# Kernel optimization log

Hardware: AMD Instinct MI355X
Metric: run time of the kernel (lower is better)

## Reference

```python
import jax, jax.numpy as jnp
import numpy as np

D_MODEL, EMB_DIM, MLP_ORDER, SEQ_LEN, BATCH = 768, 3, 16, 8192, 8


def setup_inputs() -> dict:
    key = jax.random.key(0)
    ks = jax.random.split(key, 12)
    L = SEQ_LEN
    # PositionalEmbedding buffers (deterministic, as in __init__)
    t = jnp.linspace(0.0, 1.0, L)[None, :, None]                      # [1, L, 1]
    bands = (EMB_DIM - 1) // 2                                        # = 1
    t_long = jnp.linspace(0.0, L - 1.0, L)[None, :, None]
    w = 2.0 * jnp.pi * t_long / L
    f = jnp.linspace(1e-4, bands - 1.0, bands)[None, None]
    zc = jnp.exp(-1j * f * w)
    z = jnp.concatenate([t, zc.real, zc.imag], axis=-1).astype(jnp.float32)  # [1, L, 3]
    # ExponentialModulation deltas (deterministic)
    max_decay = jnp.log(0.01) / 0.3
    min_decay = jnp.log(0.01) / 1.5
    deltas = jnp.linspace(min_decay, max_decay, D_MODEL)[None, None].astype(jnp.float32)  # [1,1,D]
    s = 0.1
    return {
        "x": jax.random.normal(ks[0], (BATCH, D_MODEL, L), jnp.float32),
        "L": L,
        "z": z,
        "t": t.astype(jnp.float32),
        "deltas": deltas,
        "freq": jnp.ones((1, MLP_ORDER), jnp.float32),
        "W0": jax.random.normal(ks[1], (EMB_DIM, MLP_ORDER), jnp.float32) * s,
        "b0": jax.random.normal(ks[2], (MLP_ORDER,), jnp.float32) * s,
        "W1": jax.random.normal(ks[3], (MLP_ORDER, MLP_ORDER), jnp.float32) * s,
        "b1": jax.random.normal(ks[4], (MLP_ORDER,), jnp.float32) * s,
        "W2": jax.random.normal(ks[5], (MLP_ORDER, MLP_ORDER), jnp.float32) * s,
        "b2": jax.random.normal(ks[6], (MLP_ORDER,), jnp.float32) * s,
        "W3": jax.random.normal(ks[7], (MLP_ORDER, D_MODEL), jnp.float32) * s,
        "b3": jax.random.normal(ks[8], (D_MODEL,), jnp.float32) * s,
        "bias": jax.random.normal(ks[9], (D_MODEL,), jnp.float32),
    }


def reference(x, L, z, t, deltas, freq, W0, b0, W1, b1, W2, b2, W3, b3, bias):
    # filter generation: MLP with shared Sin activation, then exponential modulation
    zl = z[:, :L]
    h = jnp.sin(freq * (zl @ W0 + b0))
    h = jnp.sin(freq * (h @ W1 + b1))
    h = jnp.sin(freq * (h @ W2 + b2))
    h = h @ W3 + b3                               # [1, L, D]
    h = h * jnp.exp(-t[:, :L] * jnp.abs(deltas))  # exponential modulation
    k = h[0].T                                    # [D, L]
    # fftconv: causal long convolution via zero-padded FFT + skip x*bias
    fft_size = 2 * L
    y = jnp.fft.irfft(jnp.fft.rfft(x, n=fft_size) * jnp.fft.rfft(k, n=fft_size), n=fft_size)[..., :L]
    return y + x * bias[:, None]
```

## Files before the change

### kernel.cpp

```cpp
#include <hip/hip_runtime.h>
#include <math.h>


#define LSEQ 8192
#define NCH 768
#define NBATCH 8
#define NT 512

#define OFF_TWB  0
#define OFF_TW16 1024
#define OFF_TL   5124
#define OFF_TWC  6660
#define OFF_H    10240
#define OFF_KF   141312

__device__ __forceinline__ float2 cadd(float2 a, float2 b){ return make_float2(a.x+b.x, a.y+b.y); }
__device__ __forceinline__ float2 csub(float2 a, float2 b){ return make_float2(a.x-b.x, a.y-b.y); }
__device__ __forceinline__ float2 cmul(float2 a, float2 b){ return make_float2(a.x*b.x - a.y*b.y, a.x*b.y + a.y*b.x); }
__device__ __forceinline__ float2 mni(float2 a){ return make_float2(a.y, -a.x); }

__device__ __forceinline__ void wave_sync(){
    asm volatile("s_waitcnt lgkmcnt(0)" ::: "memory");
}
__device__ __forceinline__ void fence(){
    asm volatile("" ::: "memory");
}

__device__ __forceinline__ int IDX(int i){ return i ^ (((i>>4) ^ (i>>8)) & 15); }
__device__ __forceinline__ int drev(int k){
    return ((k & 15) << 9) | (((k >> 4) & 15) << 5) | (((k >> 8) & 15) << 1) | (k >> 12);
}

#define C1 0.923879532511286756f
#define S1 0.382683432365089772f
#define R2 0.707106781186547524f

template<bool FULL>
__device__ __forceinline__ void dft16(float2 q[16]) {
    if constexpr (FULL) {
#pragma unroll
        for (int j = 0; j < 8; ++j) { float2 u=q[j], v=q[j+8]; q[j]=cadd(u,v); q[j+8]=csub(u,v); }
    }
    q[9]  = cmul(q[9],  make_float2( C1,-S1));
    q[10] = cmul(q[10], make_float2( R2,-R2));
    q[11] = cmul(q[11], make_float2( S1,-C1));
    q[12] = mni(q[12]);
    q[13] = cmul(q[13], make_float2(-S1,-C1));
    q[14] = cmul(q[14], make_float2(-R2,-R2));
    q[15] = cmul(q[15], make_float2(-C1,-S1));
#pragma unroll
    for (int b = 0; b < 16; b += 8) {
#pragma unroll
        for (int j = 0; j < 4; ++j) { float2 u=q[b+j], v=q[b+j+4]; q[b+j]=cadd(u,v); q[b+j+4]=csub(u,v); }
        q[b+5] = cmul(q[b+5], make_float2( R2,-R2));
        q[b+6] = mni(q[b+6]);
        q[b+7] = cmul(q[b+7], make_float2(-R2,-R2));
    }
#pragma unroll
    for (int b = 0; b < 16; b += 4) {
        float2 u0=q[b], v0=q[b+2], u1=q[b+1], v1=q[b+3];
        q[b]=cadd(u0,v0); q[b+2]=csub(u0,v0);
        q[b+1]=cadd(u1,v1); q[b+3]=mni(csub(u1,v1));
    }
#pragma unroll
    for (int b = 0; b < 16; b += 2) { float2 u=q[b], v=q[b+1]; q[b]=cadd(u,v); q[b+1]=csub(u,v); }
}

template<int PASS>
__device__ __forceinline__ int psb(int t) {
    if constexpr (PASS == 0) {
        return t ^ (((t>>4) ^ (t>>8)) & 15);
    } else if constexpr (PASS == 1) {
        int p = t & 31, hb = t >> 5;
        return ((hb<<9) | p) ^ (((p>>4) ^ (hb<<1)) & 15);
    } else {
        int h = t >> 1;
        return ((h<<5) | (t&1)) ^ (((h<<1) ^ (h>>3)) & 15);
    }
}
template<int PASS>
__device__ __forceinline__ int paddr(int sb, int r) {
    if constexpr (PASS == 0)      return (sb ^ (2*(r&7))) + (r<<9);
    else if constexpr (PASS == 1) return (sb ^ ((2*(r&7)) ^ (r>>3))) + (r<<5);
    else                          return sb ^ ((r<<1) ^ (r>>3));
}

template<int PASS, bool DIT, bool PRUNED>
__device__ __forceinline__ void r16p(float2* lds, const float2 (*twT)[68], int t) {
    static constexpr int RV[16] = {0,8,4,12,2,10,6,14,1,9,5,13,3,11,7,15};
    const int sb = psb<PASS>(t);
    int rL, rH = 0;
    if constexpr (PASS == 0) { rL = 32 + (t & 31); rH = (t >> 5) << 1; }
    else if constexpr (PASS == 1) { rL = t & 31; }
    else { rL = 64 + (t & 1); }
    float2 q[16];
    if constexpr (PRUNED) {
#pragma unroll
        for (int r = 0; r < 8; ++r) { q[r] = lds[paddr<PASS>(sb, r)]; q[r+8] = q[r]; }
    } else {
#pragma unroll
        for (int r = 0; r < 16; ++r) q[r] = lds[paddr<PASS>(sb, r)];
    }
    if constexpr (DIT) {
#pragma unroll
        for (int m = 1; m < 16; ++m) {
            float2 w = twT[m][rL];
            if constexpr (PASS == 0) w = cmul(w, twT[m][rH]);
            q[m] = cmul(q[m], w);
        }
        dft16<true>(q);
    } else {
        dft16<!PRUNED>(q);
#pragma unroll
        for (int m = 1; m < 16; ++m) {
            float2 w = twT[m][rL];
            if constexpr (PASS == 0) w = cmul(w, twT[m][rH]);
            q[RV[m]] = cmul(q[RV[m]], w);
        }
    }
#pragma unroll
    for (int m = 0; m < 16; ++m) lds[paddr<PASS>(sb, m)] = q[RV[m]];
}

template<int PASS, bool DIT, bool PRUNED>
__device__ __forceinline__ void r16pp(float2* l0, float2* l1, const float2 (*twT)[68], int t) {
    r16p<PASS, DIT, PRUNED>(l0, twT, t);
    fence();
    r16p<PASS, DIT, PRUNED>(l1, twT, t);
}

__device__ __forceinline__ void load_twT(float2 (*twT)[68], const float* __restrict__ ws, int tid) {
    const float2* gTWB = (const float2*)(ws + OFF_TWB);
    const float2* gTL  = (const float2*)(ws + OFF_TL);
    const float2* gTWC = (const float2*)(ws + OFF_TWC);
    for (int idx = tid; idx < 16*66; idx += NT) {
        int r = idx >> 4, m = idx & 15;
        float2 v;
        if (r < 32)      v = gTWB[(r << 4) + m];
        else if (r < 64) v = gTL[((r - 32) << 4) + m];
        else             v = gTWC[((r - 64) << 4) + m];
        twT[m][r] = v;
    }
}

__device__ __forceinline__ void specpair(float2 V1, float2 V2, float4 kv, float2 W,
                                         float2& o1, float2& o2) {
    float2 Eh = make_float2(V1.x + V2.x, V1.y - V2.y);
    float2 Oh = make_float2(V1.y + V2.y, V2.x - V1.x);
    float2 S = make_float2(kv.x, kv.y);
    float a = W.x*kv.z, b = W.y*kv.w, cc = W.x*kv.w, dd = W.y*kv.z;
    float2 T  = make_float2(a - b, cc + dd);
    float2 T2 = make_float2(a + b, cc - dd);
    float2 Ep = cadd(cmul(Eh, S), cmul(Oh, T));
    float2 Op = cadd(cmul(Eh, T2), cmul(Oh, S));
    o1 = make_float2(Ep.y + Op.x, Ep.x - Op.y);
    o2 = make_float2(Op.x - Ep.y, Ep.x + Op.y);
}

__device__ __forceinline__ void spec_rows(float2* l, int pA, int pB,
                                          float4 kvk, float4 kvj, float2 W, float2 Wj) {
    float2 uA = l[pA], vA = l[pA^1];
    float2 uB = l[pB], vB = l[pB^1];
    float2 Vk = cadd(uA, vA), Vk4 = csub(uA, vA);
    float2 Vj = cadd(uB, vB), Vj4 = csub(uB, vB);
    float2 r1, r2, r1j, r2j;
    specpair(Vk, Vj4, kvk, W,  r1,  r2);
    specpair(Vj, Vk4, kvj, Wj, r1j, r2j);
    l[pA]   = cadd(r1, r2j);  l[pA^1] = csub(r1, r2j);
    l[pB]   = cadd(r1j, r2);  l[pB^1] = csub(r1j, r2);
}

__device__ __forceinline__ void spec_dc(float2* l, float4 kv) {
    float2 u = l[0], v = l[1];
    float2 V0 = cadd(u, v), VN = csub(u, v);
    float U0 = V0.x + V0.y, UL = V0.x - V0.y;
    float re = U0*kv.x + UL*kv.y;
    float im = U0*kv.x - UL*kv.y;
    float2 s0 = make_float2(im, re);
    float2 P = make_float2(VN.x*kv.z + VN.y*kv.w, VN.x*kv.w - VN.y*kv.z);
    float2 s1 = make_float2(-P.y, P.x);
    l[0] = cadd(s0, s1);
    l[1] = csub(s0, s1);
}

__device__ __forceinline__ void filt_store(float2* l, float4* kf, int k, int jj,
                                           int pA, int pB, float2 W, float2 Wj,
                                           float sc, float eb) {
    float2 uA = l[pA], vA = l[pA^1];
    float2 uB = l[pB], vB = l[pB^1];
    float2 Vk = cadd(uA, vA), Vk4 = csub(uA, vA);
    float2 Vj = cadd(uB, vB), Vj4 = csub(uB, vB);
    {
        float2 E = make_float2(Vk.x + Vj4.x + eb, Vk.y - Vj4.y);
        float2 O = make_float2(Vk.y + Vj4.y, Vj4.x - Vk.x);
        float2 D = cmul(W, O);
        kf[k] = make_float4(E.x*sc, E.y*sc, D.x*sc, D.y*sc);
    }
    {
        float2 E = make_float2(Vj.x + Vk4.x + eb, Vj.y - Vk4.y);
        float2 O = make_float2(Vj.y + Vk4.y, Vk4.x - Vj.x);
        float2 D = cmul(Wj, O);
        kf[jj] = make_float4(E.x*sc, E.y*sc, D.x*sc, D.y*sc);
    }
}
__device__ __forceinline__ void filt_dc(float2* l, float4* kf, float bc) {
    float2 u = l[0], v = l[1];
    float2 V0 = cadd(u, v), VN = csub(u, v);
    kf[0] = make_float4((V0.x + V0.y + bc)/16384.f, (V0.x - V0.y + bc)/16384.f,
                        (VN.x + bc)/8192.f, -VN.y/8192.f);
}

__global__ __launch_bounds__(512) void k_pre(const float* __restrict__ z, const float* __restrict__ freq,
        const float* __restrict__ W0, const float* __restrict__ b0,
        const float* __restrict__ W1, const float* __restrict__ b1,
        const float* __restrict__ W2, const float* __restrict__ b2,
        float* __restrict__ ws, float* __restrict__ H) {
    __shared__ double2 lA[128], lB[128];
    const int t = threadIdx.x;
    if (blockIdx.x == 0) {
        const double K = -2.0 * 3.14159265358979323846 / 16384.0;
        if (t < 128)      { double a = K * (double)(t << 7); lA[t] = make_double2(cos(a), sin(a)); }
        else if (t < 256) { int b = t - 128; double a = K * (double)b; lB[b] = make_double2(cos(a), sin(a)); }
        __syncthreads();
        auto wf = [&](int e) -> float2 {
            e &= 16383;
            double2 A = lA[e >> 7], B = lB[e & 127];
            return make_float2((float)(A.x*B.x - A.y*B.y), (float)(A.x*B.y + A.y*B.x));
        };
        float2* tw16 = (float2*)(ws + OFF_TW16);
        for (int k = t; k <= 2048; k += 512) tw16[k] = wf(k);
        if (t < 32) {
            float2* rowL = (float2*)(ws + OFF_TL)  + (t << 4);
            float2* rowB = (float2*)(ws + OFF_TWB) + (t << 4);
#pragma unroll
            for (int m = 0; m < 16; ++m) { rowL[m] = wf(2*t*m); rowB[m] = wf(32*t*m); }
        } else if (t < 34) {
            int c2 = t - 32;
            float2* rowC = (float2*)(ws + OFF_TWC) + (c2 << 4);
#pragma unroll
            for (int m = 0; m < 16; ++m) rowC[m] = wf(512*c2*m);
        }
    } else {
        const int j = ((blockIdx.x - 1) << 9) + t;
        const float z0 = z[j*3+0], z1 = z[j*3+1], z2 = z[j*3+2];
        float h[16], g[16];
#pragma unroll
        for (int m = 0; m < 16; ++m)
            h[m] = sinf(freq[m] * (z0*W0[m] + z1*W0[16+m] + z2*W0[32+m] + b0[m]));
#pragma unroll
        for (int m = 0; m < 16; ++m) {
            float a = b1[m];
#pragma unroll
            for (int p = 0; p < 16; ++p) a += h[p] * W1[p*16+m];
            g[m] = sinf(freq[m] * a);
        }
#pragma unroll
        for (int m = 0; m < 16; ++m) {
            float a = b2[m];
#pragma unroll
            for (int p = 0; p < 16; ++p) a += g[p] * W2[p*16+m];
            h[m] = sinf(freq[m] * a);
        }
        float4* hp = (float4*)(H + (j << 4));
        hp[0] = make_float4(h[0],  h[1],  h[2],  h[3]);
        hp[1] = make_float4(h[4],  h[5],  h[6],  h[7]);
        hp[2] = make_float4(h[8],  h[9],  h[10], h[11]);
        hp[3] = make_float4(h[12], h[13], h[14], h[15]);
    }
}

__global__ __launch_bounds__(NT) void k_filter(const float* __restrict__ H, const float* __restrict__ t,
        const float* __restrict__ deltas, const float* __restrict__ W3,
        const float* __restrict__ b3, const float* __restrict__ bias,
        const float* __restrict__ ws, float* __restrict__ KfF) {
    __shared__ float2 lds2[2][LSEQ];
    __shared__ float2 twT[16][68];
    const int c0 = blockIdx.x << 1, c1 = c0 + 1;
    const int tid = threadIdx.x;
    float2* l0 = lds2[0];
    float2* l1 = lds2[1];
    load_twT(twT, ws, tid);
    float w30[16], w31[16];
#pragma unroll
    for (int m = 0; m < 16; ++m) { w30[m] = W3[m*NCH + c0]; w31[m] = W3[m*NCH + c1]; }
    const float b30 = b3[c0], b31 = b3[c1];
    const float ad0 = fabsf(deltas[c0]), ad1 = fabsf(deltas[c1]);
    const float bc0 = bias[c0], bc1 = bias[c1];
    const int sbA = psb<0>(tid);
#pragma unroll 1
    for (int j = 0; j < 8; ++j) {
        int n = tid + (j << 9);
        const float4* hp = (const float4*)(H + (n << 5));
        float sA0 = b30, sB0 = b30, sA1 = b31, sB1 = b31;
#pragma unroll
        for (int q = 0; q < 4; ++q) {
            float4 a = hp[q];
            float4 b = hp[4+q];
            sA0 += a.x*w30[4*q] + a.y*w30[4*q+1] + a.z*w30[4*q+2] + a.w*w30[4*q+3];
            sB0 += b.x*w30[4*q] + b.y*w30[4*q+1] + b.z*w30[4*q+2] + b.w*w30[4*q+3];
            sA1 += a.x*w31[4*q] + a.y*w31[4*q+1] + a.z*w31[4*q+2] + a.w*w31[4*q+3];
            sB1 += b.x*w31[4*q] + b.y*w31[4*q+1] + b.z*w31[4*q+2] + b.w*w31[4*q+3];
        }
        float2 tv = ((const float2*)t)[n];
        int a0 = (sbA ^ (2*j)) + (j<<9);
        l0[a0] = make_float2(sA0 * expf(-tv.x*ad0), sB0 * expf(-tv.y*ad0));
        l1[a0] = make_float2(sA1 * expf(-tv.x*ad1), sB1 * expf(-tv.y*ad1));
    }
    __syncthreads();
    r16pp<0,false,true >(l0, l1, twT, tid); __syncthreads();
    r16pp<1,false,false>(l0, l1, twT, tid); wave_sync();
    r16pp<2,false,false>(l0, l1, twT, tid); __syncthreads();

    float4* kf0 = (float4*)KfF + (size_t)c0 * 4096;
    float4* kf1 = (float4*)KfF + (size_t)c1 * 4096;
    const float2* tw16 = (const float2*)(ws + OFF_TW16);
    const float sc = 1.0f / 32768.0f;
#pragma unroll 1
    for (int it = 0; it < 4; ++it) {
        int k  = tid + 1 + (it << 9);
        int jj = 4096 - k;
        int pA = IDX(drev(k)), pB = IDX(drev(jj));
        float2 W  = tw16[k];
        float2 Wj = make_float2(-W.y, -W.x);
        filt_store(l0, kf0, k, jj, pA, pB, W, Wj, sc, 2.0f*bc0);
        filt_store(l1, kf1, k, jj, pA, pB, W, Wj, sc, 2.0f*bc1);
    }
    if (tid == 0) { filt_dc(l0, kf0, bc0); filt_dc(l1, kf1, bc1); }
}

__global__ __launch_bounds__(NT) void k_main(const float* __restrict__ x, const float* __restrict__ ws,
        const float* __restrict__ KfF, float* __restrict__ out) {
    __shared__ float2 lds2[2][LSEQ];
    __shared__ float2 twT[16][68];
    const int bid = blockIdx.x;
    const int c = bid >> 1, half = bid & 1;
    const int tt = threadIdx.x;
    float2* l0 = lds2[0];
    float2* l1 = lds2[1];
    const float4* kf4 = (const float4*)KfF + (size_t)c * 4096;
    const float2* tw16 = (const float2*)(ws + OFF_TW16);
    const size_t rowstride = (size_t)NCH * LSEQ;
    const float* xbase = x + (size_t)(half*4) * rowstride + (size_t)c * LSEQ;
    float* obase = out + (size_t)(half*4) * rowstride + (size_t)c * LSEQ;

    const int EB = (tt << 1) ^ (((tt>>3) ^ (tt>>7)) & 15);

    load_twT(twT, ws, tt);

#pragma unroll 1
    for (int pp = 0; pp < 2; ++pp) {
        const float4* xr0 = (const float4*)(xbase + (size_t)(2*pp)     * rowstride);
        const float4* xr1 = (const float4*)(xbase + (size_t)(2*pp + 1) * rowstride);
#pragma unroll
        for (int j = 0; j < 4; ++j) {
            float4 v0 = xr0[tt + (j<<9)];
            float4 v1 = xr1[tt + (j<<9)];
            int a0 = (EB ^ (j<<2)) + (j<<10);
            l0[a0]   = make_float2(v0.x, v0.y);
            l0[a0^1] = make_float2(v0.z, v0.w);
            l1[a0]   = make_float2(v1.x, v1.y);
            l1[a0^1] = make_float2(v1.z, v1.w);
        }
        __syncthreads();
        r16pp<0,false,true >(l0, l1, twT, tt); __syncthreads();
        r16pp<1,false,false>(l0, l1, twT, tt); wave_sync();
        r16pp<2,false,false>(l0, l1, twT, tt); __syncthreads();

#pragma unroll 1
        for (int it = 0; it < 4; ++it) {
            int k  = tt + 1 + (it << 9);
            int jj = 4096 - k;
            int pA = IDX(drev(k)), pB = IDX(drev(jj));
            float4 kvk = kf4[k], kvj = kf4[jj];
            float2 W  = tw16[k];
            float2 Wj = make_float2(-W.y, -W.x);
            spec_rows(l0, pA, pB, kvk, kvj, W, Wj);
            spec_rows(l1, pA, pB, kvk, kvj, W, Wj);
        }
        if (tt == 0) {
            float4 kv = kf4[0];
            spec_dc(l0, kv);
            spec_dc(l1, kv);
        }
        __syncthreads();

        r16pp<2,true,false>(l0, l1, twT, tt); wave_sync();
        r16pp<1,true,false>(l0, l1, twT, tt); __syncthreads();
        r16pp<0,true,false>(l0, l1, twT, tt); __syncthreads();

        float4* o0 = (float4*)(obase + (size_t)(2*pp)     * rowstride);
        float4* o1 = (float4*)(obase + (size_t)(2*pp + 1) * rowstride);
#pragma unroll
        for (int j = 0; j < 4; ++j) {
            int a0 = (EB ^ (j<<2)) + (j<<10);
            float2 wA0 = l0[a0], wB0 = l0[a0^1];
            float2 wA1 = l1[a0], wB1 = l1[a0^1];
            o0[tt + (j<<9)] = make_float4(wA0.y, wA0.x, wB0.y, wB0.x);
            o1[tt + (j<<9)] = make_float4(wA1.y, wA1.x, wB1.y, wB1.x);
        }
        if (pp == 0) __syncthreads();
    }
}

extern "C" void kernel_launch(void* const* d_in, const int* in_sizes, int n_in,
                              void* d_out, int out_size, void* d_ws, size_t ws_size,
                              hipStream_t stream) {
    const float* x      = (const float*)d_in[0];
    const float* z      = (const float*)d_in[2];
    const float* t      = (const float*)d_in[3];
    const float* deltas = (const float*)d_in[4];
    const float* freq   = (const float*)d_in[5];
    const float* W0     = (const float*)d_in[6];
    const float* b0     = (const float*)d_in[7];
    const float* W1     = (const float*)d_in[8];
    const float* b1     = (const float*)d_in[9];
    const float* W2     = (const float*)d_in[10];
    const float* b2     = (const float*)d_in[11];
    const float* W3     = (const float*)d_in[12];
    const float* b3     = (const float*)d_in[13];
    const float* bias   = (const float*)d_in[14];
    float* out = (float*)d_out;
    float* ws  = (float*)d_ws;
    float* H   = ws + OFF_H;
    float* Kf  = ws + OFF_KF;

    hipLaunchKernelGGL(k_pre, dim3(17), dim3(512), 0, stream, z, freq, W0, b0, W1, b1, W2, b2, ws, H);
    hipLaunchKernelGGL(k_filter, dim3(NCH/2), dim3(NT), 0, stream, H, t, deltas, W3, b3, bias, ws, Kf);
    hipLaunchKernelGGL(k_main, dim3(NBATCH * NCH / 4), dim3(NT), 0, stream, x, ws, Kf, out);
}
```

Measured before the change: 646.7 us.

## Pair-preserving LDS swizzle for 128-bit accesses and packed complex vector math

Changes the LDS XOR swizzle masks from 15 to 14 so adjacent complex pairs stay contiguous. Input staging, output readback, the spectral multiply and the filter store can then use float4 (128-bit) LDS accesses instead of pairs of float2 accesses. It also switches complex arithmetic to a 2-wide ext_vector type so the compiler can emit packed FP32 instructions. The narrower swizzle may bring back some LDS bank conflicts in the radix-16 passes, since their paddr formulas were simplified.

```diff
diff --git a/kernel.cpp b/kernel.cpp
--- a/kernel.cpp
+++ b/kernel.cpp
@@ -14,10 +14,14 @@
 #define OFF_H    10240
 #define OFF_KF   141312
 
-__device__ __forceinline__ float2 cadd(float2 a, float2 b){ return make_float2(a.x+b.x, a.y+b.y); }
-__device__ __forceinline__ float2 csub(float2 a, float2 b){ return make_float2(a.x-b.x, a.y-b.y); }
-__device__ __forceinline__ float2 cmul(float2 a, float2 b){ return make_float2(a.x*b.x - a.y*b.y, a.x*b.y + a.y*b.x); }
-__device__ __forceinline__ float2 mni(float2 a){ return make_float2(a.y, -a.x); }
+typedef float cplx __attribute__((ext_vector_type(2)));
+
+__device__ __forceinline__ cplx cadd(cplx a, cplx b){ return a + b; }
+__device__ __forceinline__ cplx csub(cplx a, cplx b){ return a - b; }
+__device__ __forceinline__ cplx cmul(cplx a, cplx b){
+    return cplx{a.x, a.x} * b + cplx{a.y, a.y} * cplx{-b.y, b.x};
+}
+__device__ __forceinline__ cplx mni(cplx a){ return cplx{a.y, -a.x}; }
 
 __device__ __forceinline__ void wave_sync(){
     asm volatile("s_waitcnt lgkmcnt(0)" ::: "memory");
@@ -26,7 +30,7 @@
     asm volatile("" ::: "memory");
 }
 
-__device__ __forceinline__ int IDX(int i){ return i ^ (((i>>4) ^ (i>>8)) & 15); }
+__device__ __forceinline__ int IDX14(int i){ return i ^ (((i>>4) ^ (i>>8)) & 14); }
 __device__ __forceinline__ int drev(int k){
     return ((k & 15) << 9) | (((k >> 4) & 15) << 5) | (((k >> 8) & 15) << 1) | (k >> 12);
 }
@@ -36,64 +40,64 @@
 #define R2 0.707106781186547524f
 
 template<bool FULL>
-__device__ __forceinline__ void dft16(float2 q[16]) {
+__device__ __forceinline__ void dft16(cplx q[16]) {
     if constexpr (FULL) {
 #pragma unroll
-        for (int j = 0; j < 8; ++j) { float2 u=q[j], v=q[j+8]; q[j]=cadd(u,v); q[j+8]=csub(u,v); }
-    }
-    q[9]  = cmul(q[9],  make_float2( C1,-S1));
-    q[10] = cmul(q[10], make_float2( R2,-R2));
-    q[11] = cmul(q[11], make_float2( S1,-C1));
+        for (int j = 0; j < 8; ++j) { cplx u=q[j], v=q[j+8]; q[j]=u+v; q[j+8]=u-v; }
+    }
+    q[9]  = cmul(q[9],  cplx{ C1,-S1});
+    q[10] = cmul(q[10], cplx{ R2,-R2});
+    q[11] = cmul(q[11], cplx{ S1,-C1});
     q[12] = mni(q[12]);
-    q[13] = cmul(q[13], make_float2(-S1,-C1));
-    q[14] = cmul(q[14], make_float2(-R2,-R2));
-    q[15] = cmul(q[15], make_float2(-C1,-S1));
+    q[13] = cmul(q[13], cplx{-S1,-C1});
+    q[14] = cmul(q[14], cplx{-R2,-R2});
+    q[15] = cmul(q[15], cplx{-C1,-S1});
 #pragma unroll
     for (int b = 0; b < 16; b += 8) {
 #pragma unroll
-        for (int j = 0; j < 4; ++j) { float2 u=q[b+j], v=q[b+j+4]; q[b+j]=cadd(u,v); q[b+j+4]=csub(u,v); }
-        q[b+5] = cmul(q[b+5], make_float2( R2,-R2));
+        for (int j = 0; j < 4; ++j) { cplx u=q[b+j], v=q[b+j+4]; q[b+j]=u+v; q[b+j+4]=u-v; }
+        q[b+5] = cmul(q[b+5], cplx{ R2,-R2});
         q[b+6] = mni(q[b+6]);
-        q[b+7] = cmul(q[b+7], make_float2(-R2,-R2));
+        q[b+7] = cmul(q[b+7], cplx{-R2,-R2});
     }
 #pragma unroll
     for (int b = 0; b < 16; b += 4) {
-        float2 u0=q[b], v0=q[b+2], u1=q[b+1], v1=q[b+3];
-        q[b]=cadd(u0,v0); q[b+2]=csub(u0,v0);
-        q[b+1]=cadd(u1,v1); q[b+3]=mni(csub(u1,v1));
-    }
-#pragma unroll
-    for (int b = 0; b < 16; b += 2) { float2 u=q[b], v=q[b+1]; q[b]=cadd(u,v); q[b+1]=csub(u,v); }
+        cplx u0=q[b], v0=q[b+2], u1=q[b+1], v1=q[b+3];
+        q[b]=u0+v0; q[b+2]=u0-v0;
+        q[b+1]=u1+v1; q[b+3]=mni(u1-v1);
+    }
+#pragma unroll
+    for (int b = 0; b < 16; b += 2) { cplx u=q[b], v=q[b+1]; q[b]=u+v; q[b+1]=u-v; }
 }
 
 template<int PASS>
 __device__ __forceinline__ int psb(int t) {
     if constexpr (PASS == 0) {
-        return t ^ (((t>>4) ^ (t>>8)) & 15);
+        return t ^ (((t>>4) ^ (t>>8)) & 14);
     } else if constexpr (PASS == 1) {
         int p = t & 31, hb = t >> 5;
-        return ((hb<<9) | p) ^ (((p>>4) ^ (hb<<1)) & 15);
+        return ((hb<<9) | p) ^ (((p>>4) ^ (hb<<1)) & 14);
     } else {
         int h = t >> 1;
-        return ((h<<5) | (t&1)) ^ (((h<<1) ^ (h>>3)) & 15);
+        return ((h<<5) | (t&1)) ^ (((h<<1) ^ (h>>3)) & 14);
     }
 }
 template<int PASS>
 __device__ __forceinline__ int paddr(int sb, int r) {
     if constexpr (PASS == 0)      return (sb ^ (2*(r&7))) + (r<<9);
-    else if constexpr (PASS == 1) return (sb ^ ((2*(r&7)) ^ (r>>3))) + (r<<5);
-    else                          return sb ^ ((r<<1) ^ (r>>3));
+    else if constexpr (PASS == 1) return (sb ^ (2*(r&7))) + (r<<5);
+    else                          return sb ^ (r<<1);
 }
 
 template<int PASS, bool DIT, bool PRUNED>
-__device__ __forceinline__ void r16p(float2* lds, const float2 (*twT)[68], int t) {
+__device__ __forceinline__ void r16p(cplx* lds, const cplx (*twT)[68], int t) {
     static constexpr int RV[16] = {0,8,4,12,2,10,6,14,1,9,5,13,3,11,7,15};
     const int sb = psb<PASS>(t);
     int rL, rH = 0;
     if constexpr (PASS == 0) { rL = 32 + (t & 31); rH = (t >> 5) << 1; }
     else if constexpr (PASS == 1) { rL = t & 31; }
     else { rL = 64 + (t & 1); }
-    float2 q[16];
+    cplx q[16];
     if constexpr (PRUNED) {
 #pragma unroll
         for (int r = 0; r < 8; ++r) { q[r] = lds[paddr<PASS>(sb, r)]; q[r+8] = q[r]; }
@@ -104,7 +108,7 @@
     if constexpr (DIT) {
 #pragma unroll
         for (int m = 1; m < 16; ++m) {
-            float2 w = twT[m][rL];
+            cplx w = twT[m][rL];
             if constexpr (PASS == 0) w = cmul(w, twT[m][rH]);
             q[m] = cmul(q[m], w);
         }
@@ -113,7 +117,7 @@
         dft16<!PRUNED>(q);
 #pragma unroll
         for (int m = 1; m < 16; ++m) {
-            float2 w = twT[m][rL];
+            cplx w = twT[m][rL];
             if constexpr (PASS == 0) w = cmul(w, twT[m][rH]);
             q[RV[m]] = cmul(q[RV[m]], w);
         }
@@ -123,19 +127,19 @@
 }
 
 template<int PASS, bool DIT, bool PRUNED>
-__device__ __forceinline__ void r16pp(float2* l0, float2* l1, const float2 (*twT)[68], int t) {
+__device__ __forceinline__ void r16pp(cplx* l0, cplx* l1, const cplx (*twT)[68], int t) {
     r16p<PASS, DIT, PRUNED>(l0, twT, t);
     fence();
     r16p<PASS, DIT, PRUNED>(l1, twT, t);
 }
 
-__device__ __forceinline__ void load_twT(float2 (*twT)[68], const float* __restrict__ ws, int tid) {
-    const float2* gTWB = (const float2*)(ws + OFF_TWB);
-    const float2* gTL  = (const float2*)(ws + OFF_TL);
-    const float2* gTWC = (const float2*)(ws + OFF_TWC);
+__device__ __forceinline__ void load_twT(cplx (*twT)[68], const float* __restrict__ ws, int tid) {
+    const cplx* gTWB = (const cplx*)(ws + OFF_TWB);
+    const cplx* gTL  = (const cplx*)(ws + OFF_TL);
+    const cplx* gTWC = (const cplx*)(ws + OFF_TWC);
     for (int idx = tid; idx < 16*66; idx += NT) {
         int r = idx >> 4, m = idx & 15;
-        float2 v;
+        cplx v;
         if (r < 32)      v = gTWB[(r << 4) + m];
         else if (r < 64) v = gTL[((r - 32) << 4) + m];
         else             v = gTWC[((r - 64) << 4) + m];
@@ -143,69 +147,75 @@
     }
 }
 
-__device__ __forceinline__ void specpair(float2 V1, float2 V2, float4 kv, float2 W,
-                                         float2& o1, float2& o2) {
-    float2 Eh = make_float2(V1.x + V2.x, V1.y - V2.y);
-    float2 Oh = make_float2(V1.y + V2.y, V2.x - V1.x);
-    float2 S = make_float2(kv.x, kv.y);
+__device__ __forceinline__ void specpair(cplx V1, cplx V2, float4 kv, cplx W,
+                                         cplx& o1, cplx& o2) {
+    cplx Eh = V1 + cplx{V2.x, -V2.y};
+    cplx Oh = cplx{V1.y + V2.y, V2.x - V1.x};
+    cplx S = cplx{kv.x, kv.y};
     float a = W.x*kv.z, b = W.y*kv.w, cc = W.x*kv.w, dd = W.y*kv.z;
-    float2 T  = make_float2(a - b, cc + dd);
-    float2 T2 = make_float2(a + b, cc - dd);
-    float2 Ep = cadd(cmul(Eh, S), cmul(Oh, T));
-    float2 Op = cadd(cmul(Eh, T2), cmul(Oh, S));
-    o1 = make_float2(Ep.y + Op.x, Ep.x - Op.y);
-    o2 = make_float2(Op.x - Ep.y, Ep.x + Op.y);
-}
-
-__device__ __forceinline__ void spec_rows(float2* l, int pA, int pB,
-                                          float4 kvk, float4 kvj, float2 W, float2 Wj) {
-    float2 uA = l[pA], vA = l[pA^1];
-    float2 uB = l[pB], vB = l[pB^1];
-    float2 Vk = cadd(uA, vA), Vk4 = csub(uA, vA);
-    float2 Vj = cadd(uB, vB), Vj4 = csub(uB, vB);
-    float2 r1, r2, r1j, r2j;
+    cplx T  = cplx{a - b, cc + dd};
+    cplx T2 = cplx{a + b, cc - dd};
+    cplx Ep = cmul(Eh, S) + cmul(Oh, T);
+    cplx Op = cmul(Eh, T2) + cmul(Oh, S);
+    o1 = cplx{Ep.y + Op.x, Ep.x - Op.y};
+    o2 = cplx{Op.x - Ep.y, Ep.x + Op.y};
+}
+
+__device__ __forceinline__ void spec_rows(float4* l4, int sA, int sB,
+                                          float4 kvk, float4 kvj, cplx W, cplx Wj) {
+    float4 fA = l4[sA], fB = l4[sB];
+    cplx uA = {fA.x, fA.y}, vA = {fA.z, fA.w};
+    cplx uB = {fB.x, fB.y}, vB = {fB.z, fB.w};
+    cplx Vk = uA + vA, Vk4 = uA - vA;
+    cplx Vj = uB + vB, Vj4 = uB - vB;
+    cplx r1, r2, r1j, r2j;
     specpair(Vk, Vj4, kvk, W,  r1,  r2);
     specpair(Vj, Vk4, kvj, Wj, r1j, r2j);
-    l[pA]   = cadd(r1, r2j);  l[pA^1] = csub(r1, r2j);
-    l[pB]   = cadd(r1j, r2);  l[pB^1] = csub(r1j, r2);
-}
-
-__device__ __forceinline__ void spec_dc(float2* l, float4 kv) {
-    float2 u = l[0], v = l[1];
-    float2 V0 = cadd(u, v), VN = csub(u, v);
+    cplx a0 = r1 + r2j, a1 = r1 - r2j;
+    cplx b0 = r1j + r2, b1 = r1j - r2;
+    l4[sA] = make_float4(a0.x, a0.y, a1.x, a1.y);
+    l4[sB] = make_float4(b0.x, b0.y, b1.x, b1.y);
+}
+
+__device__ __forceinline__ void spec_dc(float4* l4, float4 kv) {
+    float4 f = l4[0];
+    cplx u = {f.x, f.y}, v = {f.z, f.w};
+    cplx V0 = u + v, VN = u - v;
     float U0 = V0.x + V0.y, UL = V0.x - V0.y;
     float re = U0*kv.x + UL*kv.y;
     float im = U0*kv.x - UL*kv.y;
-    float2 s0 = make_float2(im, re);
-    float2 P = make_float2(VN.x*kv.z + VN.y*kv.w, VN.x*kv.w - VN.y*kv.z);
-    float2 s1 = make_float2(-P.y, P.x);
-    l[0] = cadd(s0, s1);
-    l[1] = csub(s0, s1);
-}
-
-__device__ __forceinline__ void filt_store(float2* l, float4* kf, int k, int jj,
-                                           int pA, int pB, float2 W, float2 Wj,
+    cplx s0 = {im, re};
+    cplx P = {VN.x*kv.z + VN.y*kv.w, VN.x*kv.w - VN.y*kv.z};
+    cplx s1 = {-P.y, P.x};
+    cplx a = s0 + s1, b = s0 - s1;
+    l4[0] = make_float4(a.x, a.y, b.x, b.y);
+}
+
+__device__ __forceinline__ void filt_store(const float4* l4, float4* kf, int k, int jj,
+                                           int sA, int sB, cplx W, cplx Wj,
                                            float sc, float eb) {
-    float2 uA = l[pA], vA = l[pA^1];
-    float2 uB = l[pB], vB = l[pB^1];
-    float2 Vk = cadd(uA, vA), Vk4 = csub(uA, vA);
-    float2 Vj = cadd(uB, vB), Vj4 = csub(uB, vB);
+    float4 fA = l4[sA], fB = l4[sB];
+    cplx uA = {fA.x, fA.y}, vA = {fA.z, fA.w};
+    cplx uB = {fB.x, fB.y}, vB = {fB.z, fB.w};
+    cplx Vk = uA + vA, Vk4 = uA - vA;
+    cplx Vj = uB + vB, Vj4 = uB - vB;
     {
-        float2 E = make_float2(Vk.x + Vj4.x + eb, Vk.y - Vj4.y);
-        float2 O = make_float2(Vk.y + Vj4.y, Vj4.x - Vk.x);
-        float2 D = cmul(W, O);
+        cplx E = {Vk.x + Vj4.x + eb, Vk.y - Vj4.y};
+        cplx O = {Vk.y + Vj4.y, Vj4.x - Vk.x};
+        cplx D = cmul(W, O);
         kf[k] = make_float4(E.x*sc, E.y*sc, D.x*sc, D.y*sc);
     }
     {
-        float2 E = make_float2(Vj.x + Vk4.x + eb, Vj.y - Vk4.y);
-        float2 O = make_float2(Vj.y + Vk4.y, Vk4.x - Vj.x);
-        float2 D = cmul(Wj, O);
+        cplx E = {Vj.x + Vk4.x + eb, Vj.y - Vk4.y};
+        cplx O = {Vj.y + Vk4.y, Vk4.x - Vj.x};
+        cplx D = cmul(Wj, O);
         kf[jj] = make_float4(E.x*sc, E.y*sc, D.x*sc, D.y*sc);
     }
 }
-__device__ __forceinline__ void filt_dc(float2* l, float4* kf, float bc) {
-    float2 u = l[0], v = l[1];
-    float2 V0 = cadd(u, v), VN = csub(u, v);
+__device__ __forceinline__ void filt_dc(const float4* l4, float4* kf, float bc) {
+    float4 f = l4[0];
+    cplx u = {f.x, f.y}, v = {f.z, f.w};
+    cplx V0 = u + v, VN = u - v;
     kf[0] = make_float4((V0.x + V0.y + bc)/16384.f, (V0.x - V0.y + bc)/16384.f,
                         (VN.x + bc)/8192.f, -VN.y/8192.f);
 }
@@ -273,12 +283,14 @@
         const float* __restrict__ deltas, const float* __restrict__ W3,
         const float* __restrict__ b3, const float* __restrict__ bias,
         const float* __restrict__ ws, float* __restrict__ KfF) {
-    __shared__ float2 lds2[2][LSEQ];
-    __shared__ float2 twT[16][68];
+    __shared__ alignas(16) cplx lds2[2][LSEQ];
+    __shared__ cplx twT[16][68];
     const int c0 = blockIdx.x << 1, c1 = c0 + 1;
     const int tid = threadIdx.x;
-    float2* l0 = lds2[0];
-    float2* l1 = lds2[1];
+    cplx* l0 = lds2[0];
+    cplx* l1 = lds2[1];
+    float4* l04 = (float4*)l0;
+    float4* l14 = (float4*)l1;
     load_twT(twT, ws, tid);
     float w30[16], w31[16];
 #pragma unroll
@@ -302,9 +314,11 @@
             sB1 += b.x*w31[4*q] + b.y*w31[4*q+1] + b.z*w31[4*q+2] + b.w*w31[4*q+3];
         }
         float2 tv = ((const float2*)t)[n];
-        int a0 = (sbA ^ (2*j)) + (j<<9);
-        l0[a0] = make_float2(sA0 * expf(-tv.x*ad0), sB0 * expf(-tv.y*ad0));
-        l1[a0] = make_float2(sA1 * expf(-tv.x*ad1), sB1 * expf(-tv.y*ad1));
+        int a0 = paddr<0>(sbA, j);
+        float e0 = expf(-tv.x*ad0), e1 = expf(-tv.y*ad0);
+        float e2 = expf(-tv.x*ad1), e3 = expf(-tv.y*ad1);
+        l0[a0] = cplx{sA0 * e0, sB0 * e1};
+        l1[a0] = cplx{sA1 * e2, sB1 * e3};
     }
     __syncthreads();
     r16pp<0,false,true >(l0, l1, twT, tid); __syncthreads();
@@ -313,37 +327,39 @@
 
     float4* kf0 = (float4*)KfF + (size_t)c0 * 4096;
     float4* kf1 = (float4*)KfF + (size_t)c1 * 4096;
-    const float2* tw16 = (const float2*)(ws + OFF_TW16);
+    const cplx* tw16 = (const cplx*)(ws + OFF_TW16);
     const float sc = 1.0f / 32768.0f;
 #pragma unroll 1
     for (int it = 0; it < 4; ++it) {
         int k  = tid + 1 + (it << 9);
         int jj = 4096 - k;
-        int pA = IDX(drev(k)), pB = IDX(drev(jj));
-        float2 W  = tw16[k];
-        float2 Wj = make_float2(-W.y, -W.x);
-        filt_store(l0, kf0, k, jj, pA, pB, W, Wj, sc, 2.0f*bc0);
-        filt_store(l1, kf1, k, jj, pA, pB, W, Wj, sc, 2.0f*bc1);
-    }
-    if (tid == 0) { filt_dc(l0, kf0, bc0); filt_dc(l1, kf1, bc1); }
+        int sA = IDX14(drev(k)) >> 1, sB = IDX14(drev(jj)) >> 1;
+        cplx W  = tw16[k];
+        cplx Wj = cplx{-W.y, -W.x};
+        filt_store(l04, kf0, k, jj, sA, sB, W, Wj, sc, 2.0f*bc0);
+        filt_store(l14, kf1, k, jj, sA, sB, W, Wj, sc, 2.0f*bc1);
+    }
+    if (tid == 0) { filt_dc(l04, kf0, bc0); filt_dc(l14, kf1, bc1); }
 }
 
 __global__ __launch_bounds__(NT) void k_main(const float* __restrict__ x, const float* __restrict__ ws,
         const float* __restrict__ KfF, float* __restrict__ out) {
-    __shared__ float2 lds2[2][LSEQ];
-    __shared__ float2 twT[16][68];
+    __shared__ alignas(16) cplx lds2[2][LSEQ];
+    __shared__ cplx twT[16][68];
     const int bid = blockIdx.x;
     const int c = bid >> 1, half = bid & 1;
     const int tt = threadIdx.x;
-    float2* l0 = lds2[0];
-    float2* l1 = lds2[1];
+    cplx* l0 = lds2[0];
+    cplx* l1 = lds2[1];
+    float4* l04 = (float4*)l0;
+    float4* l14 = (float4*)l1;
     const float4* kf4 = (const float4*)KfF + (size_t)c * 4096;
-    const float2* tw16 = (const float2*)(ws + OFF_TW16);
+    const cplx* tw16 = (const cplx*)(ws + OFF_TW16);
     const size_t rowstride = (size_t)NCH * LSEQ;
     const float* xbase = x + (size_t)(half*4) * rowstride + (size_t)c * LSEQ;
     float* obase = out + (size_t)(half*4) * rowstride + (size_t)c * LSEQ;
 
-    const int EB = (tt << 1) ^ (((tt>>3) ^ (tt>>7)) & 15);
+    const int EB = (tt << 1) ^ (((tt>>3) ^ (tt>>7)) & 14);
 
     load_twT(twT, ws, tt);
 
@@ -353,13 +369,9 @@
         const float4* xr1 = (const float4*)(xbase + (size_t)(2*pp + 1) * rowstride);
 #pragma unroll
         for (int j = 0; j < 4; ++j) {
-            float4 v0 = xr0[tt + (j<<9)];
-            float4 v1 = xr1[tt + (j<<9)];
-            int a0 = (EB ^ (j<<2)) + (j<<10);
-            l0[a0]   = make_float2(v0.x, v0.y);
-            l0[a0^1] = make_float2(v0.z, v0.w);
-            l1[a0]   = make_float2(v1.x, v1.y);
-            l1[a0^1] = make_float2(v1.z, v1.w);
+            int si = ((EB ^ (j<<2)) + (j<<10)) >> 1;
+            l04[si] = xr0[tt + (j<<9)];
+            l14[si] = xr1[tt + (j<<9)];
         }
         __syncthreads();
         r16pp<0,false,true >(l0, l1, twT, tt); __syncthreads();
@@ -370,17 +382,17 @@
         for (int it = 0; it < 4; ++it) {
             int k  = tt + 1 + (it << 9);
             int jj = 4096 - k;
-            int pA = IDX(drev(k)), pB = IDX(drev(jj));
+            int sA = IDX14(drev(k)) >> 1, sB = IDX14(drev(jj)) >> 1;
             float4 kvk = kf4[k], kvj = kf4[jj];
-            float2 W  = tw16[k];
-            float2 Wj = make_float2(-W.y, -W.x);
-            spec_rows(l0, pA, pB, kvk, kvj, W, Wj);
-            spec_rows(l1, pA, pB, kvk, kvj, W, Wj);
+            cplx W  = tw16[k];
+            cplx Wj = cplx{-W.y, -W.x};
+            spec_rows(l04, sA, sB, kvk, kvj, W, Wj);
+            spec_rows(l14, sA, sB, kvk, kvj, W, Wj);
         }
         if (tt == 0) {
             float4 kv = kf4[0];
-            spec_dc(l0, kv);
-            spec_dc(l1, kv);
+            spec_dc(l04, kv);
+            spec_dc(l14, kv);
         }
         __syncthreads();
 
@@ -392,11 +404,10 @@
         float4* o1 = (float4*)(obase + (size_t)(2*pp + 1) * rowstride);
 #pragma unroll
         for (int j = 0; j < 4; ++j) {
-            int a0 = (EB ^ (j<<2)) + (j<<10);
-            float2 wA0 = l0[a0], wB0 = l0[a0^1];
-            float2 wA1 = l1[a0], wB1 = l1[a0^1];
-            o0[tt + (j<<9)] = make_float4(wA0.y, wA0.x, wB0.y, wB0.x);
-            o1[tt + (j<<9)] = make_float4(wA1.y, wA1.x, wB1.y, wB1.x);
+            int si = ((EB ^ (j<<2)) + (j<<10)) >> 1;
+            float4 f0 = l04[si], f1 = l14[si];
+            o0[tt + (j<<9)] = make_float4(f0.y, f0.x, f0.w, f0.z);
+            o1[tt + (j<<9)] = make_float4(f1.y, f1.x, f1.w, f1.z);
         }
         if (pp == 0) __syncthreads();
     }
```

After: 607.9 us. 6.0% less time.
